# Performance work log

Hardware: AMD Instinct MI355X
Metric: run time of the kernel (lower is better)

Reference implementation:

```python
import jax, jax.numpy as jnp
import numpy as np

NEG = -1000000000.0
EPS = 1e-05

def setup_inputs() -> dict:
    key = jax.random.key(0)
    k1, k2, k3, k4, k5 = jax.random.split(key, 5)
    B, L, E, Q = 64, 2048, 512, 256
    encoded_vecs = jax.random.normal(k1, (B, L, E), dtype=jnp.float32)
    query = jax.random.normal(k2, (B, Q), dtype=jnp.float32)
    length = jax.random.randint(k3, (B,), 1, L + 1, dtype=jnp.int32)
    # Xavier-normal-ish params
    W1 = jax.random.normal(k4, (E + Q, E), dtype=jnp.float32) * jnp.sqrt(2.0 / (E + Q + E))
    b1 = jnp.zeros((E,), dtype=jnp.float32)
    v = jax.random.normal(k5, (E,), dtype=jnp.float32) * jnp.sqrt(2.0 / (E + 1))
    return {"encoded_vecs": encoded_vecs, "query": query, "length": length,
            "W1": W1, "b1": b1, "v": v}

def reference(encoded_vecs, query, length, W1, b1, v):
    B, L, E = encoded_vecs.shape
    # broadcast 2D query over the length dim (repeat in torch code)
    q = jnp.broadcast_to(query[:, None, :], (B, L, query.shape[-1]))
    h = jnp.concatenate([encoded_vecs, q], axis=2)            # [B, L, E+Q]
    u = jnp.tanh(jnp.einsum('blc,ce->ble', h, W1) + b1)       # [B, L, E]
    logits = jnp.einsum('ble,e->bl', u, v)                    # [B, L]
    # masked softmax (faithful to masked_softmax in source)
    mask = (jnp.arange(L)[None, :] < length[:, None])         # [B, L] bool
    masked_logits = jnp.where(mask, logits, NEG)
    max_logits = jnp.max(masked_logits, axis=1, keepdims=True)
    exps = jnp.exp(masked_logits - max_logits) * mask.astype(logits.dtype)
    attention = exps / (jnp.sum(exps, axis=1, keepdims=True) + EPS)  # [B, L]
    context = jnp.einsum('bl,ble->be', attention, encoded_vecs)      # [B, E]
    return (context, attention)
```

## Files before the change

kernel.cpp:

```cpp
#include <hip/hip_runtime.h>

typedef __attribute__((ext_vector_type(4))) float float4v;
typedef __attribute__((ext_vector_type(2))) float float2v;
typedef __attribute__((ext_vector_type(8))) short short8;
typedef __attribute__((ext_vector_type(4))) float f32x4;

#define NEGV (-1000000000.0f)

#define MTOT (64 * 2048)

__device__ __forceinline__ unsigned short f2bf(float f) {
    unsigned int u = __float_as_uint(f);
    u += 0x7fffu + ((u >> 16) & 1u);
    return (unsigned short)(u >> 16);
}

__device__ __forceinline__ void gload_lds16(const void* g, void* l) {
    __builtin_amdgcn_global_load_lds(
        (__attribute__((address_space(1))) unsigned int*)(unsigned long long)(g),
        (__attribute__((address_space(3))) unsigned int*)(unsigned int)(unsigned long long)(l),
        16, 0, 0);
}

__global__ __launch_bounds__(256)
void prep_wt_kernel(const float* __restrict__ W1, unsigned short* __restrict__ Wt,
                    float* __restrict__ ctxraw, float* __restrict__ S) {
    __shared__ float t[32][33];
    int blk = blockIdx.x;
    if (threadIdx.x < 128) ctxraw[blk * 128 + threadIdx.x] = 0.f;
    if (blk == 0 && threadIdx.x >= 128 && threadIdx.x < 192) S[threadIdx.x - 128] = 0.f;
    int bx = blk & 15;
    int by = blk >> 4;
    int tx = threadIdx.x & 31;
    int ty = threadIdx.x >> 5;
    #pragma unroll
    for (int i = 0; i < 4; ++i)
        t[ty + 8 * i][tx] = W1[(bx * 32 + ty + 8 * i) * 512 + by * 32 + tx];
    __syncthreads();
    #pragma unroll
    for (int i = 0; i < 4; ++i)
        Wt[(by * 32 + ty + 8 * i) * 512 + bx * 32 + tx] = f2bf(t[tx][ty + 8 * i]);
}

__global__ __launch_bounds__(256)
void prep_qc_kernel(const float* __restrict__ query, const float* __restrict__ W1,
                    const float* __restrict__ b1, float* __restrict__ qc) {
    __shared__ float part[128];
    int blk = blockIdx.x;
    int b = blk >> 2;
    int e = (blk & 3) * 128 + (threadIdx.x & 127);
    int qh = threadIdx.x >> 7;
    const float* w = W1 + (512 + qh * 128) * 512;
    const float* qv = query + b * 256 + qh * 128;
    float acc = 0.f;
    #pragma unroll 8
    for (int q = 0; q < 128; ++q)
        acc += qv[q] * w[q * 512 + e];
    if (qh) part[threadIdx.x & 127] = acc;
    __syncthreads();
    if (!qh) qc[b * 512 + e] = b1[e] + acc + part[threadIdx.x & 127];
}

__global__ __launch_bounds__(1024)
void gemm_fused_kernel(const float* __restrict__ A,
                       const unsigned short* __restrict__ Wt,
                       const float* __restrict__ qc,
                       const float* __restrict__ v,
                       const int* __restrict__ length,
                       float* __restrict__ att,
                       float* __restrict__ ctxraw,
                       float* __restrict__ S)
{
    int bm = blockIdx.x;
    int b = bm >> 4;
    int len = length[b];
    int l0 = (bm & 15) * 128;
    if (l0 >= len) return;

    __shared__ char smem[147456];
    unsigned short* As = (unsigned short*)smem;
    unsigned short* Bs = (unsigned short*)(smem + 16384);
    float (*lred)[8] = (float(*)[8])(smem + 16384);
    float* wbuf = (float*)(smem + 16384 + 4096);

    int tid = threadIdx.x;
    int lane = tid & 63;
    int w = tid >> 6;
    int wm = w >> 3, wn = w & 7;
    long row0 = (long)bm * 128;

    int ar_r = tid >> 3;
    int ar_e = tid & 7;
    const char* gAr = (const char*)A + (row0 + ar_r) * 2048 + ar_e * 16;
    int awr = ar_r * 64 + ((ar_e * 8) ^ (((ar_r >> 1) & 3) << 4));

    int offw = w * 2048 + lane * 16;
    const char* gB0;
    const char* gB1;
    {
        int o = offw;
        int r = o >> 6;
        gB0 = (const char*)Wt + r * 1024 + ((o & 63) ^ (((r >> 1) & 3) << 4));
        o = offw + 1024;
        r = o >> 6;
        gB1 = (const char*)Wt + r * 1024 + ((o & 63) ^ (((r >> 1) & 3) << 4));
    }

    int aoff[4], boff[4];
    int kb = 16 * (lane >> 4);
    #pragma unroll
    for (int mi = 0; mi < 4; ++mi) {
        int ar = wm * 64 + (lane & 15) + mi * 16;
        aoff[mi] = ar * 64 + (kb ^ (((ar >> 1) & 3) << 4));
    }
    #pragma unroll
    for (int ni = 0; ni < 4; ++ni) {
        int br = wn * 64 + (lane & 15) + ni * 16;
        boff[ni] = br * 64 + (kb ^ (((br >> 1) & 3) << 4));
    }

    f32x4 acc[4][4] = {};
    float4v Pa, Pb, Pc, Pd;

#define ALOAD(t_, P_) do { P_ = *(const float4v*)(gAr + (t_) * 128); } while (0)

#define BISSUE(t_, sI) do {                                                  \
    char* lb_ = (char*)Bs + (sI) * 32768 + offw;                             \
    gload_lds16(gB0 + (t_) * 64, lb_);                                       \
    gload_lds16(gB1 + (t_) * 64, lb_ + 1024);                                \
} while (0)

#define CVTW(P_, sW) do {                                                    \
    union { unsigned int u[2]; unsigned long long ll; } pk_;                 \
    pk_.u[0] = (unsigned int)f2bf(P_[0]) | ((unsigned int)f2bf(P_[1]) << 16); \
    pk_.u[1] = (unsigned int)f2bf(P_[2]) | ((unsigned int)f2bf(P_[3]) << 16); \
    *(unsigned long long*)((char*)As + (sW) * 8192 + awr) = pk_.ll;          \
} while (0)

#define KCOMP(sA, sB) do {                                                   \
    const char* as_ = (const char*)As + (sA) * 8192;                         \
    const char* bs_ = (const char*)Bs + (sB) * 32768;                        \
    short8 af_[4];                                                           \
    _Pragma("unroll")                                                        \
    for (int mi = 0; mi < 4; ++mi) af_[mi] = *(const short8*)(as_ + aoff[mi]); \
    _Pragma("unroll")                                                        \
    for (int ni = 0; ni < 4; ++ni) {                                         \
        short8 bf_ = *(const short8*)(bs_ + boff[ni]);                       \
        _Pragma("unroll")                                                    \
        for (int mi = 0; mi < 4; ++mi)                                       \
            acc[mi][ni] = __builtin_amdgcn_mfma_f32_16x16x32_bf16(af_[mi], bf_, acc[mi][ni], 0, 0, 0); \
    }                                                                        \
} while (0)

#define PHASE(p, PI0, PI1, PC0, PC1, AISS, VM) do {                          \
    BISSUE(2*(p)+2, (2*(p)+2) & 3);                                          \
    BISSUE(2*(p)+3, (2*(p)+3) & 3);                                          \
    if (AISS) { ALOAD(2*(p)+4, PI0); ALOAD(2*(p)+5, PI1); }                  \
    KCOMP(0, (2*(p)) & 3);                                                   \
    KCOMP(1, (2*(p)+1) & 3);                                                 \
    asm volatile("" ::: "memory");                                           \
    __builtin_amdgcn_s_barrier();                                            \
    asm volatile("s_waitcnt vmcnt(" #VM ")" ::: "memory");                   \
    CVTW(PC0, 0);                                                            \
    CVTW(PC1, 1);                                                            \
    asm volatile("s_waitcnt lgkmcnt(0)" ::: "memory");                       \
    __builtin_amdgcn_s_barrier();                                            \
    asm volatile("" ::: "memory");                                           \
} while (0)

    ALOAD(0, Pa);
    ALOAD(1, Pb);
    BISSUE(0, 0);
    BISSUE(1, 1);
    ALOAD(2, Pc);
    ALOAD(3, Pd);
    asm volatile("s_waitcnt vmcnt(2)" ::: "memory");
    CVTW(Pa, 0);
    CVTW(Pb, 1);
    asm volatile("s_waitcnt lgkmcnt(0)" ::: "memory");
    __builtin_amdgcn_s_barrier();
    asm volatile("" ::: "memory");

    PHASE(0, Pa, Pb, Pc, Pd, 1, 2);
    PHASE(1, Pc, Pd, Pa, Pb, 1, 2);
    PHASE(2, Pa, Pb, Pc, Pd, 1, 2);
    PHASE(3, Pc, Pd, Pa, Pb, 1, 2);
    PHASE(4, Pa, Pb, Pc, Pd, 1, 2);
    PHASE(5, Pc, Pd, Pa, Pb, 1, 2);
    PHASE(6, Pa, Pb, Pc, Pd, 0, 0);
    KCOMP(0, 2);
    KCOMP(1, 3);

    const float* qcb = qc + b * 512;
    float vcol[4], qcol[4];
    #pragma unroll
    for (int ni = 0; ni < 4; ++ni) {
        int c = wn * 64 + ni * 16 + (lane & 15);
        vcol[ni] = v[c];
        qcol[ni] = qcb[c];
    }
    #pragma unroll
    for (int mi = 0; mi < 4; ++mi) {
        #pragma unroll
        for (int j2 = 0; j2 < 4; ++j2) {
            float s = 0.f;
            #pragma unroll
            for (int ni = 0; ni < 4; ++ni) {
                float xx = acc[mi][ni][j2] + qcol[ni];
                float e2 = __expf(2.0f * xx);
                float tt = 1.0f - 2.0f * __builtin_amdgcn_rcpf(e2 + 1.0f);
                s += tt * vcol[ni];
            }
            s += __shfl_xor(s, 1);
            s += __shfl_xor(s, 2);
            s += __shfl_xor(s, 4);
            s += __shfl_xor(s, 8);
            if ((lane & 15) == 0)
                lred[wm * 64 + mi * 16 + 4 * (lane >> 4) + j2][wn] = s;
        }
    }
    __syncthreads();

    if (tid < 128) {
        float lg = 0.f;
        #pragma unroll
        for (int q = 0; q < 8; ++q) lg += lred[tid][q];
        float wf = (l0 + tid < len) ? __expf(lg) : 0.f;
        att[row0 + tid] = wf;
        wbuf[tid] = wf;
        float s = wf;
        #pragma unroll
        for (int m = 32; m; m >>= 1) s += __shfl_xor(s, m);
        if ((tid & 63) == 0) atomicAdd(&S[b], s);
    }
    __syncthreads();

    {
        int e = tid & 511;
        int lh = tid >> 9;
        const float* encb = A + (row0 + lh * 64) * 512 + e;
        const float* wb = &wbuf[lh * 64];
        float c = 0.f;
        #pragma unroll 4
        for (int l = 0; l < 64; ++l)
            c += wb[l] * encb[l * 512];
        atomicAdd(&ctxraw[b * 512 + e], c);
    }
}

__global__ void norm_kernel(const float* __restrict__ S, const int* __restrict__ length,
                            const float* __restrict__ ctxraw,
                            float* __restrict__ att, float* __restrict__ ctx) {
    int b = blockIdx.x;
    int tid = threadIdx.x;
    float inv = 1.0f / S[b];
    ctx[b * 512 + tid] = ctxraw[b * 512 + tid] * inv;
    ctx[b * 512 + 256 + tid] = ctxraw[b * 512 + 256 + tid] * inv;
    int len = length[b];
    float* ab = att + b * 2048;
    #pragma unroll
    for (int i = 0; i < 8; ++i) {
        int l = tid + i * 256;
        float wv = ab[l];
        ab[l] = (l < len) ? wv * inv : 0.f;
    }
}

extern "C" void kernel_launch(void* const* d_in, const int* in_sizes, int n_in,
                              void* d_out, int out_size, void* d_ws, size_t ws_size,
                              hipStream_t stream) {
    const float* enc    = (const float*)d_in[0];
    const float* query  = (const float*)d_in[1];
    const int*   length = (const int*)d_in[2];
    const float* W1     = (const float*)d_in[3];
    const float* b1     = (const float*)d_in[4];
    const float* v      = (const float*)d_in[5];

    float* out = (float*)d_out;
    float* ctx = out;
    float* att = out + 64 * 512;

    char* ws = (char*)d_ws;
    float* qc          = (float*)ws;
    unsigned short* Wt = (unsigned short*)(ws + 64 * 512 * 4);
    float* ctxraw      = (float*)(ws + 64 * 512 * 4 + 512 * 1024);
    float* S           = (float*)(ws + 64 * 512 * 4 + 512 * 1024 + 64 * 512 * 4);

    prep_wt_kernel<<<256, 256, 0, stream>>>(W1, Wt, ctxraw, S);
    prep_qc_kernel<<<256, 256, 0, stream>>>(query, W1, b1, qc);

    gemm_fused_kernel<<<1024, 1024, 0, stream>>>(enc, Wt, qc, v, length, att, ctxraw, S);

    norm_kernel<<<64, 256, 0, stream>>>(S, length, ctxraw, att, ctx);
}
```

Baseline: 126.5 us.

## Retile fused GEMM to 64-row blocks with whole A tile preloaded in LDS

Tiles shrink from 128 to 64 rows of the sequence, giving 2048 blocks of 512 threads. The whole 64x512 bf16 A tile is converted and stored in LDS once up front. Each wave owns a 64-column slice of W and streams it through its own 3-stage LDS ring, so the main loop has no block-wide barriers. Finer tiles also skip more masked-out rows past each sequence length. In exchange, each W tile is fetched by twice as many blocks, LDS use grows to 160KB, the A loads no longer overlap compute, and ctx/S atomics double.

```diff
diff --git a/kernel.cpp b/kernel.cpp
--- a/kernel.cpp
+++ b/kernel.cpp
@@ -1,11 +1,8 @@
 #include <hip/hip_runtime.h>
 
 typedef __attribute__((ext_vector_type(4))) float float4v;
-typedef __attribute__((ext_vector_type(2))) float float2v;
 typedef __attribute__((ext_vector_type(8))) short short8;
 typedef __attribute__((ext_vector_type(4))) float f32x4;
-
-#define NEGV (-1000000000.0f)
 
 #define MTOT (64 * 2048)
 
@@ -61,7 +58,7 @@
     if (!qh) qc[b * 512 + e] = b1[e] + acc + part[threadIdx.x & 127];
 }
 
-__global__ __launch_bounds__(1024)
+__global__ __launch_bounds__(512)
 void gemm_fused_kernel(const float* __restrict__ A,
                        const unsigned short* __restrict__ Wt,
                        const float* __restrict__ qc,
@@ -72,74 +69,90 @@
                        float* __restrict__ S)
 {
     int bm = blockIdx.x;
-    int b = bm >> 4;
+    int b = bm >> 5;
     int len = length[b];
-    int l0 = (bm & 15) * 128;
+    int l0 = (bm & 31) * 64;
     if (l0 >= len) return;
 
-    __shared__ char smem[147456];
+    __shared__ char smem[163840];
     unsigned short* As = (unsigned short*)smem;
-    unsigned short* Bs = (unsigned short*)(smem + 16384);
-    float (*lred)[8] = (float(*)[8])(smem + 16384);
-    float* wbuf = (float*)(smem + 16384 + 4096);
+    float (*lred)[8] = (float(*)[8])smem;
+    float* wbuf = (float*)(smem + 2048);
 
     int tid = threadIdx.x;
     int lane = tid & 63;
     int w = tid >> 6;
-    int wm = w >> 3, wn = w & 7;
-    long row0 = (long)bm * 128;
-
-    int ar_r = tid >> 3;
-    int ar_e = tid & 7;
-    const char* gAr = (const char*)A + (row0 + ar_r) * 2048 + ar_e * 16;
-    int awr = ar_r * 64 + ((ar_e * 8) ^ (((ar_r >> 1) & 3) << 4));
-
-    int offw = w * 2048 + lane * 16;
-    const char* gB0;
-    const char* gB1;
-    {
-        int o = offw;
+    long row0 = (long)bm * 64;
+    char* myB = smem + 65536 + w * 12288;
+
+    const char* gBsrc[4];
+    int bls[4];
+    #pragma unroll
+    for (int i = 0; i < 4; ++i) {
+        int o = i * 1024 + lane * 16;
         int r = o >> 6;
-        gB0 = (const char*)Wt + r * 1024 + ((o & 63) ^ (((r >> 1) & 3) << 4));
-        o = offw + 1024;
-        r = o >> 6;
-        gB1 = (const char*)Wt + r * 1024 + ((o & 63) ^ (((r >> 1) & 3) << 4));
+        bls[i] = o;
+        gBsrc[i] = (const char*)Wt + (long)(w * 64 + r) * 1024
+                 + ((o & 63) ^ (((r >> 1) & 3) << 4));
     }
 
     int aoff[4], boff[4];
     int kb = 16 * (lane >> 4);
     #pragma unroll
     for (int mi = 0; mi < 4; ++mi) {
-        int ar = wm * 64 + (lane & 15) + mi * 16;
+        int ar = mi * 16 + (lane & 15);
         aoff[mi] = ar * 64 + (kb ^ (((ar >> 1) & 3) << 4));
     }
     #pragma unroll
     for (int ni = 0; ni < 4; ++ni) {
-        int br = wn * 64 + (lane & 15) + ni * 16;
+        int br = ni * 16 + (lane & 15);
         boff[ni] = br * 64 + (kb ^ (((br >> 1) & 3) << 4));
     }
 
+#define BISSUE(t_, sI) do {                                                  \
+    char* lb_ = myB + (sI) * 4096;                                           \
+    gload_lds16(gBsrc[0] + (t_) * 64, lb_ + bls[0]);                         \
+    gload_lds16(gBsrc[1] + (t_) * 64, lb_ + bls[1]);                         \
+    gload_lds16(gBsrc[2] + (t_) * 64, lb_ + bls[2]);                         \
+    gload_lds16(gBsrc[3] + (t_) * 64, lb_ + bls[3]);                         \
+} while (0)
+
+    BISSUE(0, 0);
+    BISSUE(1, 1);
+
+    {
+        int r = tid >> 3;
+        int e8 = tid & 7;
+        const float* gA = A + (row0 + r) * 512 + e8 * 64;
+        int swz = ((r >> 1) & 3) << 4;
+        #pragma unroll
+        for (int i = 0; i < 4; ++i) {
+            float4v x0 = *(const float4v*)(gA + i * 16);
+            float4v x1 = *(const float4v*)(gA + i * 16 + 4);
+            float4v x2 = *(const float4v*)(gA + i * 16 + 8);
+            float4v x3 = *(const float4v*)(gA + i * 16 + 12);
+            union { unsigned int u[4]; short8 s; } p0, p1;
+            p0.u[0] = (unsigned int)f2bf(x0[0]) | ((unsigned int)f2bf(x0[1]) << 16);
+            p0.u[1] = (unsigned int)f2bf(x0[2]) | ((unsigned int)f2bf(x0[3]) << 16);
+            p0.u[2] = (unsigned int)f2bf(x1[0]) | ((unsigned int)f2bf(x1[1]) << 16);
+            p0.u[3] = (unsigned int)f2bf(x1[2]) | ((unsigned int)f2bf(x1[3]) << 16);
+            p1.u[0] = (unsigned int)f2bf(x2[0]) | ((unsigned int)f2bf(x2[1]) << 16);
+            p1.u[1] = (unsigned int)f2bf(x2[2]) | ((unsigned int)f2bf(x2[3]) << 16);
+            p1.u[2] = (unsigned int)f2bf(x3[0]) | ((unsigned int)f2bf(x3[1]) << 16);
+            p1.u[3] = (unsigned int)f2bf(x3[2]) | ((unsigned int)f2bf(x3[3]) << 16);
+            int st = e8 * 2 + (i >> 1);
+            int b0 = (i & 1) * 32;
+            *(short8*)((char*)As + st * 4096 + r * 64 + (b0 ^ swz)) = p0.s;
+            *(short8*)((char*)As + st * 4096 + r * 64 + ((b0 + 16) ^ swz)) = p1.s;
+        }
+    }
+    __syncthreads();
+
     f32x4 acc[4][4] = {};
-    float4v Pa, Pb, Pc, Pd;
-
-#define ALOAD(t_, P_) do { P_ = *(const float4v*)(gAr + (t_) * 128); } while (0)
-
-#define BISSUE(t_, sI) do {                                                  \
-    char* lb_ = (char*)Bs + (sI) * 32768 + offw;                             \
-    gload_lds16(gB0 + (t_) * 64, lb_);                                       \
-    gload_lds16(gB1 + (t_) * 64, lb_ + 1024);                                \
-} while (0)
-
-#define CVTW(P_, sW) do {                                                    \
-    union { unsigned int u[2]; unsigned long long ll; } pk_;                 \
-    pk_.u[0] = (unsigned int)f2bf(P_[0]) | ((unsigned int)f2bf(P_[1]) << 16); \
-    pk_.u[1] = (unsigned int)f2bf(P_[2]) | ((unsigned int)f2bf(P_[3]) << 16); \
-    *(unsigned long long*)((char*)As + (sW) * 8192 + awr) = pk_.ll;          \
-} while (0)
-
-#define KCOMP(sA, sB) do {                                                   \
-    const char* as_ = (const char*)As + (sA) * 8192;                         \
-    const char* bs_ = (const char*)Bs + (sB) * 32768;                        \
+
+#define KCOMP(tA, sB) do {                                                   \
+    const char* as_ = (const char*)As + (tA) * 4096;                         \
+    const char* bs_ = (const char*)myB + (sB) * 4096;                        \
     short8 af_[4];                                                           \
     _Pragma("unroll")                                                        \
     for (int mi = 0; mi < 4; ++mi) af_[mi] = *(const short8*)(as_ + aoff[mi]); \
@@ -152,53 +165,26 @@
     }                                                                        \
 } while (0)
 
-#define PHASE(p, PI0, PI1, PC0, PC1, AISS, VM) do {                          \
-    BISSUE(2*(p)+2, (2*(p)+2) & 3);                                          \
-    BISSUE(2*(p)+3, (2*(p)+3) & 3);                                          \
-    if (AISS) { ALOAD(2*(p)+4, PI0); ALOAD(2*(p)+5, PI1); }                  \
-    KCOMP(0, (2*(p)) & 3);                                                   \
-    KCOMP(1, (2*(p)+1) & 3);                                                 \
-    asm volatile("" ::: "memory");                                           \
-    __builtin_amdgcn_s_barrier();                                            \
+#define STEP(t, BISS, VM) do {                                               \
+    if (BISS) BISSUE((t) + 2, ((t) + 2) % 3);                                \
     asm volatile("s_waitcnt vmcnt(" #VM ")" ::: "memory");                   \
-    CVTW(PC0, 0);                                                            \
-    CVTW(PC1, 1);                                                            \
-    asm volatile("s_waitcnt lgkmcnt(0)" ::: "memory");                       \
-    __builtin_amdgcn_s_barrier();                                            \
-    asm volatile("" ::: "memory");                                           \
+    KCOMP(t, (t) % 3);                                                       \
 } while (0)
 
-    ALOAD(0, Pa);
-    ALOAD(1, Pb);
-    BISSUE(0, 0);
-    BISSUE(1, 1);
-    ALOAD(2, Pc);
-    ALOAD(3, Pd);
-    asm volatile("s_waitcnt vmcnt(2)" ::: "memory");
-    CVTW(Pa, 0);
-    CVTW(Pb, 1);
-    asm volatile("s_waitcnt lgkmcnt(0)" ::: "memory");
-    __builtin_amdgcn_s_barrier();
-    asm volatile("" ::: "memory");
-
-    PHASE(0, Pa, Pb, Pc, Pd, 1, 2);
-    PHASE(1, Pc, Pd, Pa, Pb, 1, 2);
-    PHASE(2, Pa, Pb, Pc, Pd, 1, 2);
-    PHASE(3, Pc, Pd, Pa, Pb, 1, 2);
-    PHASE(4, Pa, Pb, Pc, Pd, 1, 2);
-    PHASE(5, Pc, Pd, Pa, Pb, 1, 2);
-    PHASE(6, Pa, Pb, Pc, Pd, 0, 0);
-    KCOMP(0, 2);
-    KCOMP(1, 3);
+    STEP(0, 1, 8);  STEP(1, 1, 8);  STEP(2, 1, 8);  STEP(3, 1, 8);
+    STEP(4, 1, 8);  STEP(5, 1, 8);  STEP(6, 1, 8);  STEP(7, 1, 8);
+    STEP(8, 1, 8);  STEP(9, 1, 8);  STEP(10, 1, 8); STEP(11, 1, 8);
+    STEP(12, 1, 8); STEP(13, 1, 8); STEP(14, 0, 4); STEP(15, 0, 0);
 
     const float* qcb = qc + b * 512;
     float vcol[4], qcol[4];
     #pragma unroll
     for (int ni = 0; ni < 4; ++ni) {
-        int c = wn * 64 + ni * 16 + (lane & 15);
+        int c = w * 64 + ni * 16 + (lane & 15);
         vcol[ni] = v[c];
         qcol[ni] = qcb[c];
     }
+    float rsum[4][4];
     #pragma unroll
     for (int mi = 0; mi < 4; ++mi) {
         #pragma unroll
@@ -215,13 +201,19 @@
             s += __shfl_xor(s, 2);
             s += __shfl_xor(s, 4);
             s += __shfl_xor(s, 8);
+            rsum[mi][j2] = s;
+        }
+    }
+    __syncthreads();
+    #pragma unroll
+    for (int mi = 0; mi < 4; ++mi)
+        #pragma unroll
+        for (int j2 = 0; j2 < 4; ++j2)
             if ((lane & 15) == 0)
-                lred[wm * 64 + mi * 16 + 4 * (lane >> 4) + j2][wn] = s;
-        }
-    }
-    __syncthreads();
-
-    if (tid < 128) {
+                lred[mi * 16 + 4 * (lane >> 4) + j2][w] = rsum[mi][j2];
+    __syncthreads();
+
+    if (tid < 64) {
         float lg = 0.f;
         #pragma unroll
         for (int q = 0; q < 8; ++q) lg += lred[tid][q];
@@ -231,20 +223,17 @@
         float s = wf;
         #pragma unroll
         for (int m = 32; m; m >>= 1) s += __shfl_xor(s, m);
-        if ((tid & 63) == 0) atomicAdd(&S[b], s);
+        if (tid == 0) atomicAdd(&S[b], s);
     }
     __syncthreads();
 
     {
-        int e = tid & 511;
-        int lh = tid >> 9;
-        const float* encb = A + (row0 + lh * 64) * 512 + e;
-        const float* wb = &wbuf[lh * 64];
+        const float* encb = A + row0 * 512 + tid;
         float c = 0.f;
         #pragma unroll 4
         for (int l = 0; l < 64; ++l)
-            c += wb[l] * encb[l * 512];
-        atomicAdd(&ctxraw[b * 512 + e], c);
+            c += wbuf[l] * encb[l * 512];
+        atomicAdd(&ctxraw[b * 512 + tid], c);
     }
 }
 
@@ -289,7 +278,7 @@
     prep_wt_kernel<<<256, 256, 0, stream>>>(W1, Wt, ctxraw, S);
     prep_qc_kernel<<<256, 256, 0, stream>>>(query, W1, b1, qc);
 
-    gemm_fused_kernel<<<1024, 1024, 0, stream>>>(enc, Wt, qc, v, length, att, ctxraw, S);
+    gemm_fused_kernel<<<2048, 512, 0, stream>>>(enc, Wt, qc, v, length, att, ctxraw, S);
 
     norm_kernel<<<64, 256, 0, stream>>>(S, length, ctxraw, att, ctx);
 }
```

After: 170.6 us. 34.9% more time.

## Read bf16 weight fragments directly from global memory instead of staging in LDS

Applied to the files above, without the earlier changes.

The transposed bf16 weight tile is no longer copied into shared memory with global_load_lds. Each wave now loads its B fragments straight from global memory (relying on L2 for reuse) inside the MFMA loop. The A staging becomes a double-buffered 4-slot ring with a single barrier per phase instead of two. This cuts LDS use from 144KB to about 37KB and removes B-side barrier and waitcnt overhead. In exchange, every MFMA step now waits on global-memory latency with no explicit prefetch, and the same weights are fetched redundantly by the many waves and blocks.

```diff
diff --git a/kernel.cpp b/kernel.cpp
--- a/kernel.cpp
+++ b/kernel.cpp
@@ -1,11 +1,8 @@
 #include <hip/hip_runtime.h>
 
 typedef __attribute__((ext_vector_type(4))) float float4v;
-typedef __attribute__((ext_vector_type(2))) float float2v;
 typedef __attribute__((ext_vector_type(8))) short short8;
 typedef __attribute__((ext_vector_type(4))) float f32x4;
-
-#define NEGV (-1000000000.0f)
 
 #define MTOT (64 * 2048)
 
@@ -13,13 +10,6 @@
     unsigned int u = __float_as_uint(f);
     u += 0x7fffu + ((u >> 16) & 1u);
     return (unsigned short)(u >> 16);
-}
-
-__device__ __forceinline__ void gload_lds16(const void* g, void* l) {
-    __builtin_amdgcn_global_load_lds(
-        (__attribute__((address_space(1))) unsigned int*)(unsigned long long)(g),
-        (__attribute__((address_space(3))) unsigned int*)(unsigned int)(unsigned long long)(l),
-        16, 0, 0);
 }
 
 __global__ __launch_bounds__(256)
@@ -77,11 +67,9 @@
     int l0 = (bm & 15) * 128;
     if (l0 >= len) return;
 
-    __shared__ char smem[147456];
-    unsigned short* As = (unsigned short*)smem;
-    unsigned short* Bs = (unsigned short*)(smem + 16384);
-    float (*lred)[8] = (float(*)[8])(smem + 16384);
-    float* wbuf = (float*)(smem + 16384 + 4096);
+    __shared__ unsigned short As[4 * 4096];
+    __shared__ float lred[128][8];
+    __shared__ float wbuf[128];
 
     int tid = threadIdx.x;
     int lane = tid & 63;
@@ -94,41 +82,25 @@
     const char* gAr = (const char*)A + (row0 + ar_r) * 2048 + ar_e * 16;
     int awr = ar_r * 64 + ((ar_e * 8) ^ (((ar_r >> 1) & 3) << 4));
 
-    int offw = w * 2048 + lane * 16;
-    const char* gB0;
-    const char* gB1;
-    {
-        int o = offw;
-        int r = o >> 6;
-        gB0 = (const char*)Wt + r * 1024 + ((o & 63) ^ (((r >> 1) & 3) << 4));
-        o = offw + 1024;
-        r = o >> 6;
-        gB1 = (const char*)Wt + r * 1024 + ((o & 63) ^ (((r >> 1) & 3) << 4));
-    }
-
-    int aoff[4], boff[4];
+    const char* gBf[4];
+    #pragma unroll
+    for (int ni = 0; ni < 4; ++ni)
+        gBf[ni] = (const char*)Wt
+                + (long)(wn * 64 + ni * 16 + (lane & 15)) * 1024
+                + (lane >> 4) * 16;
+
+    int aoff[4];
     int kb = 16 * (lane >> 4);
     #pragma unroll
     for (int mi = 0; mi < 4; ++mi) {
         int ar = wm * 64 + (lane & 15) + mi * 16;
         aoff[mi] = ar * 64 + (kb ^ (((ar >> 1) & 3) << 4));
     }
-    #pragma unroll
-    for (int ni = 0; ni < 4; ++ni) {
-        int br = wn * 64 + (lane & 15) + ni * 16;
-        boff[ni] = br * 64 + (kb ^ (((br >> 1) & 3) << 4));
-    }
 
     f32x4 acc[4][4] = {};
     float4v Pa, Pb, Pc, Pd;
 
 #define ALOAD(t_, P_) do { P_ = *(const float4v*)(gAr + (t_) * 128); } while (0)
-
-#define BISSUE(t_, sI) do {                                                  \
-    char* lb_ = (char*)Bs + (sI) * 32768 + offw;                             \
-    gload_lds16(gB0 + (t_) * 64, lb_);                                       \
-    gload_lds16(gB1 + (t_) * 64, lb_ + 1024);                                \
-} while (0)
 
 #define CVTW(P_, sW) do {                                                    \
     union { unsigned int u[2]; unsigned long long ll; } pk_;                 \
@@ -137,32 +109,27 @@
     *(unsigned long long*)((char*)As + (sW) * 8192 + awr) = pk_.ll;          \
 } while (0)
 
-#define KCOMP(sA, sB) do {                                                   \
+#define KCOMP(sA, t_) do {                                                   \
     const char* as_ = (const char*)As + (sA) * 8192;                         \
-    const char* bs_ = (const char*)Bs + (sB) * 32768;                        \
     short8 af_[4];                                                           \
     _Pragma("unroll")                                                        \
     for (int mi = 0; mi < 4; ++mi) af_[mi] = *(const short8*)(as_ + aoff[mi]); \
     _Pragma("unroll")                                                        \
     for (int ni = 0; ni < 4; ++ni) {                                         \
-        short8 bf_ = *(const short8*)(bs_ + boff[ni]);                       \
+        short8 bf_ = *(const short8*)(gBf[ni] + (t_) * 64);                  \
         _Pragma("unroll")                                                    \
         for (int mi = 0; mi < 4; ++mi)                                       \
             acc[mi][ni] = __builtin_amdgcn_mfma_f32_16x16x32_bf16(af_[mi], bf_, acc[mi][ni], 0, 0, 0); \
     }                                                                        \
 } while (0)
 
-#define PHASE(p, PI0, PI1, PC0, PC1, AISS, VM) do {                          \
-    BISSUE(2*(p)+2, (2*(p)+2) & 3);                                          \
-    BISSUE(2*(p)+3, (2*(p)+3) & 3);                                          \
+#define PHASE(p, PI0, PI1, PC0, PC1, AISS) do {                              \
+    KCOMP(2*((p)&1),     2*(p));                                             \
+    KCOMP(2*((p)&1) + 1, 2*(p)+1);                                           \
+    asm volatile("" ::: "memory");                                           \
     if (AISS) { ALOAD(2*(p)+4, PI0); ALOAD(2*(p)+5, PI1); }                  \
-    KCOMP(0, (2*(p)) & 3);                                                   \
-    KCOMP(1, (2*(p)+1) & 3);                                                 \
-    asm volatile("" ::: "memory");                                           \
-    __builtin_amdgcn_s_barrier();                                            \
-    asm volatile("s_waitcnt vmcnt(" #VM ")" ::: "memory");                   \
-    CVTW(PC0, 0);                                                            \
-    CVTW(PC1, 1);                                                            \
+    CVTW(PC0, 2*(((p)+1)&1));                                                \
+    CVTW(PC1, 2*(((p)+1)&1) + 1);                                            \
     asm volatile("s_waitcnt lgkmcnt(0)" ::: "memory");                       \
     __builtin_amdgcn_s_barrier();                                            \
     asm volatile("" ::: "memory");                                           \
@@ -170,26 +137,23 @@
 
     ALOAD(0, Pa);
     ALOAD(1, Pb);
-    BISSUE(0, 0);
-    BISSUE(1, 1);
     ALOAD(2, Pc);
     ALOAD(3, Pd);
-    asm volatile("s_waitcnt vmcnt(2)" ::: "memory");
     CVTW(Pa, 0);
     CVTW(Pb, 1);
     asm volatile("s_waitcnt lgkmcnt(0)" ::: "memory");
     __builtin_amdgcn_s_barrier();
     asm volatile("" ::: "memory");
 
-    PHASE(0, Pa, Pb, Pc, Pd, 1, 2);
-    PHASE(1, Pc, Pd, Pa, Pb, 1, 2);
-    PHASE(2, Pa, Pb, Pc, Pd, 1, 2);
-    PHASE(3, Pc, Pd, Pa, Pb, 1, 2);
-    PHASE(4, Pa, Pb, Pc, Pd, 1, 2);
-    PHASE(5, Pc, Pd, Pa, Pb, 1, 2);
-    PHASE(6, Pa, Pb, Pc, Pd, 0, 0);
-    KCOMP(0, 2);
-    KCOMP(1, 3);
+    PHASE(0, Pa, Pb, Pc, Pd, 1);
+    PHASE(1, Pc, Pd, Pa, Pb, 1);
+    PHASE(2, Pa, Pb, Pc, Pd, 1);
+    PHASE(3, Pc, Pd, Pa, Pb, 1);
+    PHASE(4, Pa, Pb, Pc, Pd, 1);
+    PHASE(5, Pc, Pd, Pa, Pb, 1);
+    PHASE(6, Pa, Pb, Pc, Pd, 0);
+    KCOMP(2, 14);
+    KCOMP(3, 15);
 
     const float* qcb = qc + b * 512;
     float vcol[4], qcol[4];
```

Result: slower. 197.3 us (+56.0%).
